# Kernel optimization log

Hardware: AMD Instinct MI355X
Metric: run time of the kernel (lower is better)

## Reference

```python
import jax, jax.numpy as jnp
import numpy as np

N_NODES = 50000


def _sage_mean(x, src, dst, Wl, bl, Wr, n_nodes):
    # PyG SAGEConv (aggr='mean', root_weight=True): lin_l(mean_j x_j) + lin_r(x_i)
    msgs = x[src]                                             # [E, F] gather
    agg = jax.ops.segment_sum(msgs, dst, num_segments=n_nodes)  # [N, F]
    cnt = jax.ops.segment_sum(jnp.ones((src.shape[0],), x.dtype), dst,
                              num_segments=n_nodes)           # [N]
    mean = agg / jnp.maximum(cnt, 1.0)[:, None]
    return mean @ Wl + bl + x @ Wr


def setup_inputs() -> dict:
    key = jax.random.key(0)
    ks = jax.random.split(key, 12)
    in_ft = 64
    o0, o1, o2 = 64, 128, 128
    d2 = o0 + o0          # conv2 in = 128
    d3 = o0 + o0 + o1     # conv3 in = 256
    E = 800000

    def lin(k, fi, fo):
        s = 1.0 / np.sqrt(fi)
        return jax.random.uniform(k, (fi, fo), jnp.float32, -s, s)

    x = jax.random.normal(ks[0], (N_NODES, in_ft), jnp.float32)
    edge_index = jax.random.randint(ks[1], (2, E), 0, N_NODES, jnp.int64)
    return {
        "x": x,
        "edge_index": edge_index,
        "Wp": lin(ks[2], in_ft, o0), "bp": jnp.zeros((o0,), jnp.float32),
        "Wl1": lin(ks[3], in_ft, o0), "bl1": jnp.zeros((o0,), jnp.float32),
        "Wr1": lin(ks[4], in_ft, o0),
        "Wl2": lin(ks[5], d2, o1), "bl2": jnp.zeros((o1,), jnp.float32),
        "Wr2": lin(ks[6], d2, o1),
        "Wl3": lin(ks[7], d3, o2), "bl3": jnp.zeros((o2,), jnp.float32),
        "Wr3": lin(ks[8], d3, o2),
    }


def reference(x, edge_index, Wp, bp, Wl1, bl1, Wr1, Wl2, bl2, Wr2, Wl3, bl3, Wr3):
    src, dst = edge_index[0], edge_index[1]
    act = jax.nn.relu
    x_p = act(x @ Wp + bp)                                        # [N, o0]
    h1 = act(_sage_mean(x, src, dst, Wl1, bl1, Wr1, N_NODES))      # [N, o0]
    in2 = jnp.concatenate([x_p, h1], axis=1)                      # [N, 2*o0]
    h2 = act(_sage_mean(in2, src, dst, Wl2, bl2, Wr2, N_NODES))    # [N, o1]
    in3 = jnp.concatenate([x_p, h1, h2], axis=1)                  # [N, 2*o0+o1]
    h3 = act(_sage_mean(in3, src, dst, Wl3, bl3, Wr3, N_NODES))    # [N, o2]
    return h3
```

## Files before the change

kernel.cpp:

```cpp
#include <hip/hip_runtime.h>

#define N_NODES 50000
#define ELLW 48

typedef unsigned int uint;
typedef unsigned short ushort;
typedef float floatx4 __attribute__((ext_vector_type(4)));
typedef short short8 __attribute__((ext_vector_type(8)));

__device__ inline ushort f2bf(float f) {
    uint u = __float_as_uint(f);
    return (ushort)((u + 0x7fffu + ((u >> 16) & 1u)) >> 16);
}
__device__ inline float bflo(uint u) { return __uint_as_float(u << 16); }
__device__ inline float bfhi(uint u) { return __uint_as_float(u & 0xffff0000u); }


__device__ inline void swz_body(const float* __restrict__ W, ushort* __restrict__ Wz,
                                int O, int t) {
    int lane = t & 63, cb = t >> 6;
    int NBm = O / 16;
    int c = cb / NBm, nb = cb % NBm;
    int quad = lane >> 4, l16 = lane & 15;
#pragma unroll
    for (int j = 0; j < 8; j++) {
        float v = W[(size_t)(c * 32 + quad * 8 + j) * O + nb * 16 + l16];
        Wz[(size_t)t * 8 + j] = f2bf(v);
    }
}

__device__ void gemm1_body(int gb, const float* __restrict__ x,
                           const float* __restrict__ Wp, const float* __restrict__ bp,
                           ushort* __restrict__ feats, ushort* ldsA) {
    constexpr int LDA = 40;
    const int tid = threadIdx.x;
    const int wave = tid >> 6, lane = tid & 63;
    const int quad = lane >> 4, l16 = lane & 15;
    const int node0 = gb * 64;

    floatx4 acc[4];
#pragma unroll
    for (int nb = 0; nb < 4; nb++) acc[nb] = (floatx4){0.f, 0.f, 0.f, 0.f};

#pragma unroll
    for (int kk = 0; kk < 2; kk++) {
        const int k0 = kk * 32;
        __syncthreads();
        {
            int row = tid >> 2, seg = tid & 3;
            int node = node0 + row;
            float4 v0 = {0.f,0.f,0.f,0.f}, v1 = {0.f,0.f,0.f,0.f};
            if (node < N_NODES) {
                v0 = *(const float4*)&x[(size_t)node * 64 + k0 + seg * 8];
                v1 = *(const float4*)&x[(size_t)node * 64 + k0 + seg * 8 + 4];
            }
            ushort4 o0, o1;
            o0.x = f2bf(v0.x); o0.y = f2bf(v0.y); o0.z = f2bf(v0.z); o0.w = f2bf(v0.w);
            o1.x = f2bf(v1.x); o1.y = f2bf(v1.y); o1.z = f2bf(v1.z); o1.w = f2bf(v1.w);
            *(ushort4*)&ldsA[row * LDA + seg * 8] = o0;
            *(ushort4*)&ldsA[row * LDA + seg * 8 + 4] = o1;
        }
        __syncthreads();

        short8 a = *(const short8*)&ldsA[(wave * 16 + l16) * LDA + quad * 8];
#pragma unroll
        for (int nb = 0; nb < 4; nb++) {
            short8 bfrag;
#pragma unroll
            for (int j = 0; j < 8; j++)
                bfrag[j] = (short)f2bf(Wp[(size_t)(k0 + quad * 8 + j) * 64 + nb * 16 + l16]);
            acc[nb] = __builtin_amdgcn_mfma_f32_16x16x32_bf16(a, bfrag, acc[nb], 0, 0, 0);
        }
    }

#pragma unroll
    for (int nb = 0; nb < 4; nb++) {
        int ncol = nb * 16 + l16;
        float bv = bp[ncol];
#pragma unroll
        for (int r = 0; r < 4; r++) {
            int node = node0 + wave * 16 + quad * 4 + r;
            if (node >= N_NODES) continue;
            float v = fmaxf(acc[nb][r] + bv, 0.f);
            feats[(size_t)node * 256 + ncol] = f2bf(v);
        }
    }
}

__global__ __launch_bounds__(256) void k1_mega(
    const int* __restrict__ src, const int* __restrict__ dst, int E,
    int* __restrict__ fillc, ushort* __restrict__ ell,
    const float* __restrict__ x, ushort* __restrict__ xb,
    const float* __restrict__ Wp, const float* __restrict__ bp, ushort* __restrict__ feats,
    const float* __restrict__ Wl1, ushort* __restrict__ zl1,
    const float* __restrict__ Wr1, ushort* __restrict__ zr1,
    const float* __restrict__ Wl2, ushort* __restrict__ zl2,
    const float* __restrict__ Wr2, ushort* __restrict__ zr2,
    const float* __restrict__ Wl3, ushort* __restrict__ zl3,
    const float* __restrict__ Wr3, ushort* __restrict__ zr3,
    int NF, int NG, int NC)
{
    __shared__ ushort ldsA[64 * 40];
    int b = blockIdx.x, tid = threadIdx.x;
    if (b < NF) {
        int t = b * 256 + tid;
        if (t < E) {
            int d = dst[t], s = src[t];
            int p = atomicAdd(&fillc[d], 1);
            if (p < ELLW) ell[(size_t)d * ELLW + p] = (ushort)s;
        }
        return;
    }
    b -= NF;
    if (b < NG) { gemm1_body(b, x, Wp, bp, feats, ldsA); return; }
    b -= NG;
    if (b < NC) {
        int t = b * 256 + tid;
        float4 v = ((const float4*)x)[t];
        ushort4 o;
        o.x = f2bf(v.x); o.y = f2bf(v.y); o.z = f2bf(v.z); o.w = f2bf(v.w);
        ((ushort4*)xb)[t] = o;
        return;
    }
    b -= NC;
    if      (b < 2)  swz_body(Wl1, zl1, 64,  (b - 0) * 256 + tid);
    else if (b < 4)  swz_body(Wr1, zr1, 64,  (b - 2) * 256 + tid);
    else if (b < 12) swz_body(Wl2, zl2, 128, (b - 4) * 256 + tid);
    else if (b < 20) swz_body(Wr2, zr2, 128, (b - 12) * 256 + tid);
    else if (b < 36) swz_body(Wl3, zl3, 128, (b - 20) * 256 + tid);
    else             swz_body(Wr3, zr3, 128, (b - 36) * 256 + tid);
}


__global__ __launch_bounds__(256) void gather64_k(const int* __restrict__ fillc,
                                                  const ushort* __restrict__ ell,
                                                  const ushort* __restrict__ in, int sin,
                                                  ushort* __restrict__ out, int sout) {
    int node = blockIdx.x * 4 + (threadIdx.x >> 6);
    if (node >= N_NODES) return;
    int lane = threadIdx.x & 63;
    int sub = lane >> 3, c = lane & 7;
    int n = fillc[node]; int nc = (n > ELLW) ? ELLW : n;
    const ushort* base = ell + (size_t)node * ELLW;
    float a[8];
#pragma unroll
    for (int j = 0; j < 8; j++) a[j] = 0.f;

    int i = sub;
    for (; i + 8 < nc; i += 16) {
        uint4 u0 = *(const uint4*)&in[(size_t)base[i] * sin + 8 * c];
        uint4 u1 = *(const uint4*)&in[(size_t)base[i + 8] * sin + 8 * c];
        a[0] += bflo(u0.x) + bflo(u1.x);  a[1] += bfhi(u0.x) + bfhi(u1.x);
        a[2] += bflo(u0.y) + bflo(u1.y);  a[3] += bfhi(u0.y) + bfhi(u1.y);
        a[4] += bflo(u0.z) + bflo(u1.z);  a[5] += bfhi(u0.z) + bfhi(u1.z);
        a[6] += bflo(u0.w) + bflo(u1.w);  a[7] += bfhi(u0.w) + bfhi(u1.w);
    }
    if (i < nc) {
        uint4 u0 = *(const uint4*)&in[(size_t)base[i] * sin + 8 * c];
        a[0] += bflo(u0.x);  a[1] += bfhi(u0.x);
        a[2] += bflo(u0.y);  a[3] += bfhi(u0.y);
        a[4] += bflo(u0.z);  a[5] += bfhi(u0.z);
        a[6] += bflo(u0.w);  a[7] += bfhi(u0.w);
    }
#pragma unroll
    for (int d = 8; d < 64; d <<= 1)
#pragma unroll
        for (int j = 0; j < 8; j++) a[j] += __shfl_xor(a[j], d);
    if (sub == 0) {
        float iv = 1.0f / fmaxf((float)n, 1.0f);
        uint4 r;
        r.x = (uint)f2bf(a[0] * iv) | ((uint)f2bf(a[1] * iv) << 16);
        r.y = (uint)f2bf(a[2] * iv) | ((uint)f2bf(a[3] * iv) << 16);
        r.z = (uint)f2bf(a[4] * iv) | ((uint)f2bf(a[5] * iv) << 16);
        r.w = (uint)f2bf(a[6] * iv) | ((uint)f2bf(a[7] * iv) << 16);
        *(uint4*)&out[(size_t)node * sout + 8 * c] = r;
    }
}

__global__ __launch_bounds__(256) void gather128_k(const int* __restrict__ fillc,
                                                   const ushort* __restrict__ ell,
                                                   const ushort* __restrict__ in, int sin,
                                                   ushort* __restrict__ out, int sout) {
    int node = blockIdx.x * 4 + (threadIdx.x >> 6);
    if (node >= N_NODES) return;
    int lane = threadIdx.x & 63;
    int sub = lane >> 4, c = lane & 15;
    int n = fillc[node]; int nc = (n > ELLW) ? ELLW : n;
    const ushort* base = ell + (size_t)node * ELLW;
    float a[8];
#pragma unroll
    for (int j = 0; j < 8; j++) a[j] = 0.f;

    int i = sub;
    for (; i + 12 < nc; i += 16) {
        uint4 u0 = *(const uint4*)&in[(size_t)base[i] * sin + 8 * c];
        uint4 u1 = *(const uint4*)&in[(size_t)base[i + 4] * sin + 8 * c];
        uint4 u2 = *(const uint4*)&in[(size_t)base[i + 8] * sin + 8 * c];
        uint4 u3 = *(const uint4*)&in[(size_t)base[i + 12] * sin + 8 * c];
        a[0] += (bflo(u0.x) + bflo(u1.x)) + (bflo(u2.x) + bflo(u3.x));
        a[1] += (bfhi(u0.x) + bfhi(u1.x)) + (bfhi(u2.x) + bfhi(u3.x));
        a[2] += (bflo(u0.y) + bflo(u1.y)) + (bflo(u2.y) + bflo(u3.y));
        a[3] += (bfhi(u0.y) + bfhi(u1.y)) + (bfhi(u2.y) + bfhi(u3.y));
        a[4] += (bflo(u0.z) + bflo(u1.z)) + (bflo(u2.z) + bflo(u3.z));
        a[5] += (bfhi(u0.z) + bfhi(u1.z)) + (bfhi(u2.z) + bfhi(u3.z));
        a[6] += (bflo(u0.w) + bflo(u1.w)) + (bflo(u2.w) + bflo(u3.w));
        a[7] += (bfhi(u0.w) + bfhi(u1.w)) + (bfhi(u2.w) + bfhi(u3.w));
    }
    for (; i < nc; i += 4) {
        uint4 u0 = *(const uint4*)&in[(size_t)base[i] * sin + 8 * c];
        a[0] += bflo(u0.x);  a[1] += bfhi(u0.x);
        a[2] += bflo(u0.y);  a[3] += bfhi(u0.y);
        a[4] += bflo(u0.z);  a[5] += bfhi(u0.z);
        a[6] += bflo(u0.w);  a[7] += bfhi(u0.w);
    }
#pragma unroll
    for (int d = 16; d < 64; d <<= 1)
#pragma unroll
        for (int j = 0; j < 8; j++) a[j] += __shfl_xor(a[j], d);
    if (sub == 0) {
        float iv = 1.0f / fmaxf((float)n, 1.0f);
        uint4 r;
        r.x = (uint)f2bf(a[0] * iv) | ((uint)f2bf(a[1] * iv) << 16);
        r.y = (uint)f2bf(a[2] * iv) | ((uint)f2bf(a[3] * iv) << 16);
        r.z = (uint)f2bf(a[4] * iv) | ((uint)f2bf(a[5] * iv) << 16);
        r.w = (uint)f2bf(a[6] * iv) | ((uint)f2bf(a[7] * iv) << 16);
        *(uint4*)&out[(size_t)node * sout + 8 * c] = r;
    }
}


template <int O, bool OUT_BF16>
__global__ __launch_bounds__(256) void mfma_gemm_k(
    const ushort* __restrict__ A1, int s1, int K1, const ushort* __restrict__ Wz1,
    const ushort* __restrict__ A2, int s2, int K2, const ushort* __restrict__ Wz2,
    const float* __restrict__ bias, void* __restrict__ outp, int so, int ocol)
{
    constexpr int NB = O / 16;
    constexpr int LDA = 40;
    __shared__ ushort ldsA[64 * LDA];

    const int tid = threadIdx.x;
    const int wave = tid >> 6, lane = tid & 63;
    const int quad = lane >> 4, l16 = lane & 15;
    const int node0 = blockIdx.x * 64;

    floatx4 acc[NB];
#pragma unroll
    for (int nb = 0; nb < NB; nb++) acc[nb] = (floatx4){0.f, 0.f, 0.f, 0.f};

#pragma unroll 1
    for (int phase = 0; phase < 2; ++phase) {
        const ushort* A = phase ? A2 : A1;
        const ushort* Wz = phase ? Wz2 : Wz1;
        const int K = phase ? K2 : K1;
        const int sA = phase ? s2 : s1;

#pragma unroll 1
        for (int k0 = 0; k0 < K; k0 += 32) {
            __syncthreads();
            {
                int row = tid >> 2, seg = tid & 3;
                int node = node0 + row;
                uint4 v = {0u, 0u, 0u, 0u};
                if (node < N_NODES)
                    v = *(const uint4*)&A[(size_t)node * sA + k0 + seg * 8];
                *(uint4*)&ldsA[row * LDA + seg * 8] = v;
            }
            __syncthreads();

            short8 a = *(const short8*)&ldsA[(wave * 16 + l16) * LDA + quad * 8];
            const short8* bz = (const short8*)Wz + (size_t)(k0 >> 5) * NB * 64;
#pragma unroll
            for (int nb = 0; nb < NB; nb++) {
                short8 b = bz[nb * 64 + lane];
                acc[nb] = __builtin_amdgcn_mfma_f32_16x16x32_bf16(a, b, acc[nb], 0, 0, 0);
            }
        }
    }

#pragma unroll
    for (int nb = 0; nb < NB; nb++) {
        int ncol = nb * 16 + l16;
        float bv = bias[ncol];
#pragma unroll
        for (int r = 0; r < 4; r++) {
            int node = node0 + wave * 16 + quad * 4 + r;
            if (node >= N_NODES) continue;
            float v = fmaxf(acc[nb][r] + bv, 0.f);
            if (OUT_BF16)
                ((ushort*)outp)[(size_t)node * so + ocol + ncol] = f2bf(v);
            else
                ((float*)outp)[(size_t)node * so + ocol + ncol] = v;
        }
    }
}


extern "C" void kernel_launch(void* const* d_in, const int* in_sizes, int n_in,
                              void* d_out, int out_size, void* d_ws, size_t ws_size,
                              hipStream_t stream) {
    const float* x   = (const float*)d_in[0];
    const int*   ei  = (const int*)d_in[1];
    const float* Wp  = (const float*)d_in[2];
    const float* bp  = (const float*)d_in[3];
    const float* Wl1 = (const float*)d_in[4];
    const float* bl1 = (const float*)d_in[5];
    const float* Wr1 = (const float*)d_in[6];
    const float* Wl2 = (const float*)d_in[7];
    const float* bl2 = (const float*)d_in[8];
    const float* Wr2 = (const float*)d_in[9];
    const float* Wl3 = (const float*)d_in[10];
    const float* bl3 = (const float*)d_in[11];
    const float* Wr3 = (const float*)d_in[12];

    const int E = in_sizes[1] / 2;
    const int N = N_NODES;
    const int* src = ei;
    const int* dst = ei + E;

    char* p = (char*)d_ws;
    ushort* xb    = (ushort*)p;  p += (size_t)N * 64 * 2;
    ushort* feats = (ushort*)p;  p += (size_t)N * 256 * 2;
    ushort* aggx  = (ushort*)p;  p += (size_t)N * 64 * 2;
    ushort* aggf  = (ushort*)p;  p += (size_t)N * 256 * 2;
    int* fillc    = (int*)p;     p += (size_t)N * 4;
    ushort* ell   = (ushort*)p;  p += (size_t)N * ELLW * 2;
    ushort* zl1   = (ushort*)p;  p += 64 * 64 * 2;
    ushort* zr1   = (ushort*)p;  p += 64 * 64 * 2;
    ushort* zl2   = (ushort*)p;  p += 128 * 128 * 2;
    ushort* zr2   = (ushort*)p;  p += 128 * 128 * 2;
    ushort* zl3   = (ushort*)p;  p += 256 * 128 * 2;
    ushort* zr3   = (ushort*)p;  p += 256 * 128 * 2;

    hipMemsetAsync(fillc, 0, (size_t)N * sizeof(int), stream);

    const int NF = (E + 255) / 256;
    const int NG = (N + 63) / 64;
    const int NC = (N * 64 / 4) / 256;

    k1_mega<<<NF + NG + NC + 52, 256, 0, stream>>>(
        src, dst, E, fillc, ell, x, xb, Wp, bp, feats,
        Wl1, zl1, Wr1, zr1, Wl2, zl2, Wr2, zr2, Wl3, zl3, Wr3, zr3,
        NF, NG, NC);

    gather64_k<<<(N + 3) / 4, 256, 0, stream>>>(fillc, ell, xb, 64, aggx, 64);

    mfma_gemm_k<64, true><<<NG, 256, 0, stream>>>(
        aggx, 64, 64, zl1, xb, 64, 64, zr1, bl1, feats, 256, 64);

    gather128_k<<<(N + 3) / 4, 256, 0, stream>>>(fillc, ell, feats, 256, aggf, 256);

    mfma_gemm_k<128, true><<<NG, 256, 0, stream>>>(
        aggf, 256, 128, zl2, feats, 256, 128, zr2, bl2, feats, 256, 128);

    gather128_k<<<(N + 3) / 4, 256, 0, stream>>>(fillc, ell, feats + 128, 256, aggf + 128, 256);

    mfma_gemm_k<128, false><<<NG, 256, 0, stream>>>(
        aggf, 256, 256, zl3, feats, 256, 256, zr3, bl3, (float*)d_out, 128, 0);
}
```

Before: 291.4 us.

## Split SAGE GEMMs into root and aggregate parts, overlapping root GEMMs with gathers

Each SAGE layer's `lin_r(x)` term is now computed separately into an fp32 partial buffer. For layer 1 it runs inside the first mega-kernel alongside the `x_p` projection. For layers 2 and 3 it runs in the same launch as the neighbour gather, with gather blocks and GEMM blocks mixed in one grid. The final per-layer kernel then only multiplies the aggregated features by `lin_l` and adds the stored partial, bias and relu. The aim is to hide root-weight GEMM work behind the memory-bound gathers and shorten the critical path. In exchange it adds extra global traffic, because fp32 partials are written and read back for every layer.

```diff
diff --git a/kernel.cpp b/kernel.cpp
--- a/kernel.cpp
+++ b/kernel.cpp
@@ -14,7 +14,6 @@
 }
 __device__ inline float bflo(uint u) { return __uint_as_float(u << 16); }
 __device__ inline float bfhi(uint u) { return __uint_as_float(u & 0xffff0000u); }
-
 
 __device__ inline void swz_body(const float* __restrict__ W, ushort* __restrict__ Wz,
                                 int O, int t) {
@@ -31,16 +30,18 @@
 
 __device__ void gemm1_body(int gb, const float* __restrict__ x,
                            const float* __restrict__ Wp, const float* __restrict__ bp,
-                           ushort* __restrict__ feats, ushort* ldsA) {
+                           const float* __restrict__ Wr1,
+                           ushort* __restrict__ feats, float* __restrict__ P1,
+                           ushort* ldsA) {
     constexpr int LDA = 40;
     const int tid = threadIdx.x;
     const int wave = tid >> 6, lane = tid & 63;
     const int quad = lane >> 4, l16 = lane & 15;
     const int node0 = gb * 64;
 
-    floatx4 acc[4];
-#pragma unroll
-    for (int nb = 0; nb < 4; nb++) acc[nb] = (floatx4){0.f, 0.f, 0.f, 0.f};
+    floatx4 aP[4], aR[4];
+#pragma unroll
+    for (int nb = 0; nb < 4; nb++) { aP[nb] = (floatx4){0,0,0,0}; aR[nb] = (floatx4){0,0,0,0}; }
 
 #pragma unroll
     for (int kk = 0; kk < 2; kk++) {
@@ -49,7 +50,7 @@
         {
             int row = tid >> 2, seg = tid & 3;
             int node = node0 + row;
-            float4 v0 = {0.f,0.f,0.f,0.f}, v1 = {0.f,0.f,0.f,0.f};
+            float4 v0 = {0,0,0,0}, v1 = {0,0,0,0};
             if (node < N_NODES) {
                 v0 = *(const float4*)&x[(size_t)node * 64 + k0 + seg * 8];
                 v1 = *(const float4*)&x[(size_t)node * 64 + k0 + seg * 8 + 4];
@@ -65,11 +66,19 @@
         short8 a = *(const short8*)&ldsA[(wave * 16 + l16) * LDA + quad * 8];
 #pragma unroll
         for (int nb = 0; nb < 4; nb++) {
-            short8 bfrag;
+            short8 bw;
 #pragma unroll
             for (int j = 0; j < 8; j++)
-                bfrag[j] = (short)f2bf(Wp[(size_t)(k0 + quad * 8 + j) * 64 + nb * 16 + l16]);
-            acc[nb] = __builtin_amdgcn_mfma_f32_16x16x32_bf16(a, bfrag, acc[nb], 0, 0, 0);
+                bw[j] = (short)f2bf(Wp[(size_t)(k0 + quad * 8 + j) * 64 + nb * 16 + l16]);
+            aP[nb] = __builtin_amdgcn_mfma_f32_16x16x32_bf16(a, bw, aP[nb], 0, 0, 0);
+        }
+#pragma unroll
+        for (int nb = 0; nb < 4; nb++) {
+            short8 bw;
+#pragma unroll
+            for (int j = 0; j < 8; j++)
+                bw[j] = (short)f2bf(Wr1[(size_t)(k0 + quad * 8 + j) * 64 + nb * 16 + l16]);
+            aR[nb] = __builtin_amdgcn_mfma_f32_16x16x32_bf16(a, bw, aR[nb], 0, 0, 0);
         }
     }
 
@@ -81,8 +90,8 @@
         for (int r = 0; r < 4; r++) {
             int node = node0 + wave * 16 + quad * 4 + r;
             if (node >= N_NODES) continue;
-            float v = fmaxf(acc[nb][r] + bv, 0.f);
-            feats[(size_t)node * 256 + ncol] = f2bf(v);
+            feats[(size_t)node * 256 + ncol] = f2bf(fmaxf(aP[nb][r] + bv, 0.f));
+            P1[(size_t)node * 64 + ncol] = aR[nb][r];
         }
     }
 }
@@ -91,9 +100,9 @@
     const int* __restrict__ src, const int* __restrict__ dst, int E,
     int* __restrict__ fillc, ushort* __restrict__ ell,
     const float* __restrict__ x, ushort* __restrict__ xb,
-    const float* __restrict__ Wp, const float* __restrict__ bp, ushort* __restrict__ feats,
+    const float* __restrict__ Wp, const float* __restrict__ bp,
+    const float* __restrict__ Wr1, ushort* __restrict__ feats, float* __restrict__ P1,
     const float* __restrict__ Wl1, ushort* __restrict__ zl1,
-    const float* __restrict__ Wr1, ushort* __restrict__ zr1,
     const float* __restrict__ Wl2, ushort* __restrict__ zl2,
     const float* __restrict__ Wr2, ushort* __restrict__ zr2,
     const float* __restrict__ Wl3, ushort* __restrict__ zl3,
@@ -112,7 +121,7 @@
         return;
     }
     b -= NF;
-    if (b < NG) { gemm1_body(b, x, Wp, bp, feats, ldsA); return; }
+    if (b < NG) { gemm1_body(b, x, Wp, bp, Wr1, feats, P1, ldsA); return; }
     b -= NG;
     if (b < NC) {
         int t = b * 256 + tid;
@@ -124,18 +133,17 @@
     }
     b -= NC;
     if      (b < 2)  swz_body(Wl1, zl1, 64,  (b - 0) * 256 + tid);
-    else if (b < 4)  swz_body(Wr1, zr1, 64,  (b - 2) * 256 + tid);
-    else if (b < 12) swz_body(Wl2, zl2, 128, (b - 4) * 256 + tid);
-    else if (b < 20) swz_body(Wr2, zr2, 128, (b - 12) * 256 + tid);
-    else if (b < 36) swz_body(Wl3, zl3, 128, (b - 20) * 256 + tid);
-    else             swz_body(Wr3, zr3, 128, (b - 36) * 256 + tid);
+    else if (b < 10) swz_body(Wl2, zl2, 128, (b - 2) * 256 + tid);
+    else if (b < 18) swz_body(Wr2, zr2, 128, (b - 10) * 256 + tid);
+    else if (b < 34) swz_body(Wl3, zl3, 128, (b - 18) * 256 + tid);
+    else             swz_body(Wr3, zr3, 128, (b - 34) * 256 + tid);
 }
 
 
 __global__ __launch_bounds__(256) void gather64_k(const int* __restrict__ fillc,
                                                   const ushort* __restrict__ ell,
-                                                  const ushort* __restrict__ in, int sin,
-                                                  ushort* __restrict__ out, int sout) {
+                                                  const ushort* __restrict__ in,
+                                                  ushort* __restrict__ out) {
     int node = blockIdx.x * 4 + (threadIdx.x >> 6);
     if (node >= N_NODES) return;
     int lane = threadIdx.x & 63;
@@ -148,15 +156,15 @@
 
     int i = sub;
     for (; i + 8 < nc; i += 16) {
-        uint4 u0 = *(const uint4*)&in[(size_t)base[i] * sin + 8 * c];
-        uint4 u1 = *(const uint4*)&in[(size_t)base[i + 8] * sin + 8 * c];
+        uint4 u0 = *(const uint4*)&in[(size_t)base[i] * 64 + 8 * c];
+        uint4 u1 = *(const uint4*)&in[(size_t)base[i + 8] * 64 + 8 * c];
         a[0] += bflo(u0.x) + bflo(u1.x);  a[1] += bfhi(u0.x) + bfhi(u1.x);
         a[2] += bflo(u0.y) + bflo(u1.y);  a[3] += bfhi(u0.y) + bfhi(u1.y);
         a[4] += bflo(u0.z) + bflo(u1.z);  a[5] += bfhi(u0.z) + bfhi(u1.z);
         a[6] += bflo(u0.w) + bflo(u1.w);  a[7] += bfhi(u0.w) + bfhi(u1.w);
     }
     if (i < nc) {
-        uint4 u0 = *(const uint4*)&in[(size_t)base[i] * sin + 8 * c];
+        uint4 u0 = *(const uint4*)&in[(size_t)base[i] * 64 + 8 * c];
         a[0] += bflo(u0.x);  a[1] += bfhi(u0.x);
         a[2] += bflo(u0.y);  a[3] += bfhi(u0.y);
         a[4] += bflo(u0.z);  a[5] += bfhi(u0.z);
@@ -173,15 +181,15 @@
         r.y = (uint)f2bf(a[2] * iv) | ((uint)f2bf(a[3] * iv) << 16);
         r.z = (uint)f2bf(a[4] * iv) | ((uint)f2bf(a[5] * iv) << 16);
         r.w = (uint)f2bf(a[6] * iv) | ((uint)f2bf(a[7] * iv) << 16);
-        *(uint4*)&out[(size_t)node * sout + 8 * c] = r;
-    }
-}
-
-__global__ __launch_bounds__(256) void gather128_k(const int* __restrict__ fillc,
-                                                   const ushort* __restrict__ ell,
-                                                   const ushort* __restrict__ in, int sin,
-                                                   ushort* __restrict__ out, int sout) {
-    int node = blockIdx.x * 4 + (threadIdx.x >> 6);
+        *(uint4*)&out[(size_t)node * 64 + 8 * c] = r;
+    }
+}
+
+__device__ void gather128_body(int gb, const int* __restrict__ fillc,
+                               const ushort* __restrict__ ell,
+                               const ushort* __restrict__ in,
+                               ushort* __restrict__ out) {
+    int node = gb * 4 + (threadIdx.x >> 6);
     if (node >= N_NODES) return;
     int lane = threadIdx.x & 63;
     int sub = lane >> 4, c = lane & 15;
@@ -193,10 +201,10 @@
 
     int i = sub;
     for (; i + 12 < nc; i += 16) {
-        uint4 u0 = *(const uint4*)&in[(size_t)base[i] * sin + 8 * c];
-        uint4 u1 = *(const uint4*)&in[(size_t)base[i + 4] * sin + 8 * c];
-        uint4 u2 = *(const uint4*)&in[(size_t)base[i + 8] * sin + 8 * c];
-        uint4 u3 = *(const uint4*)&in[(size_t)base[i + 12] * sin + 8 * c];
+        uint4 u0 = *(const uint4*)&in[(size_t)base[i] * 256 + 8 * c];
+        uint4 u1 = *(const uint4*)&in[(size_t)base[i + 4] * 256 + 8 * c];
+        uint4 u2 = *(const uint4*)&in[(size_t)base[i + 8] * 256 + 8 * c];
+        uint4 u3 = *(const uint4*)&in[(size_t)base[i + 12] * 256 + 8 * c];
         a[0] += (bflo(u0.x) + bflo(u1.x)) + (bflo(u2.x) + bflo(u3.x));
         a[1] += (bfhi(u0.x) + bfhi(u1.x)) + (bfhi(u2.x) + bfhi(u3.x));
         a[2] += (bflo(u0.y) + bflo(u1.y)) + (bflo(u2.y) + bflo(u3.y));
@@ -207,7 +215,7 @@
         a[7] += (bfhi(u0.w) + bfhi(u1.w)) + (bfhi(u2.w) + bfhi(u3.w));
     }
     for (; i < nc; i += 4) {
-        uint4 u0 = *(const uint4*)&in[(size_t)base[i] * sin + 8 * c];
+        uint4 u0 = *(const uint4*)&in[(size_t)base[i] * 256 + 8 * c];
         a[0] += bflo(u0.x);  a[1] += bfhi(u0.x);
         a[2] += bflo(u0.y);  a[3] += bfhi(u0.y);
         a[4] += bflo(u0.z);  a[5] += bfhi(u0.z);
@@ -224,21 +232,96 @@
         r.y = (uint)f2bf(a[2] * iv) | ((uint)f2bf(a[3] * iv) << 16);
         r.z = (uint)f2bf(a[4] * iv) | ((uint)f2bf(a[5] * iv) << 16);
         r.w = (uint)f2bf(a[6] * iv) | ((uint)f2bf(a[7] * iv) << 16);
-        *(uint4*)&out[(size_t)node * sout + 8 * c] = r;
-    }
-}
-
-
-template <int O, bool OUT_BF16>
-__global__ __launch_bounds__(256) void mfma_gemm_k(
-    const ushort* __restrict__ A1, int s1, int K1, const ushort* __restrict__ Wz1,
-    const ushort* __restrict__ A2, int s2, int K2, const ushort* __restrict__ Wz2,
-    const float* __restrict__ bias, void* __restrict__ outp, int so, int ocol)
+        *(uint4*)&out[(size_t)node * 256 + 8 * c] = r;
+    }
+}
+
+__device__ void pgemm_body(int gb,
+    const ushort* __restrict__ A1, int s1, int o1, int KC1, const ushort* __restrict__ Wz1, int w1,
+    const ushort* __restrict__ A2, int s2, int o2, int KC2, const ushort* __restrict__ Wz2, int w2,
+    float* __restrict__ Pout, ushort* ldsA)
+{
+    constexpr int LDA = 40;
+    const int tid = threadIdx.x;
+    const int wave = tid >> 6, lane = tid & 63;
+    const int quad = lane >> 4, l16 = lane & 15;
+    const int node0 = gb * 64;
+
+    floatx4 acc[8];
+#pragma unroll
+    for (int nb = 0; nb < 8; nb++) acc[nb] = (floatx4){0,0,0,0};
+
+#pragma unroll 1
+    for (int ph = 0; ph < 2; ph++) {
+        const ushort* A = ph ? A2 : A1;
+        const int sA = ph ? s2 : s1, oA = ph ? o2 : o1, KC = ph ? KC2 : KC1, w = ph ? w2 : w1;
+        const short8* Wz = (const short8*)(ph ? Wz2 : Wz1);
+#pragma unroll 1
+        for (int kc = 0; kc < KC; kc++) {
+            __syncthreads();
+            {
+                int row = tid >> 2, seg = tid & 3;
+                int node = node0 + row;
+                uint4 v = {0,0,0,0};
+                if (node < N_NODES)
+                    v = *(const uint4*)&A[(size_t)node * sA + oA + kc * 32 + seg * 8];
+                *(uint4*)&ldsA[row * LDA + seg * 8] = v;
+            }
+            __syncthreads();
+            short8 a = *(const short8*)&ldsA[(wave * 16 + l16) * LDA + quad * 8];
+            const short8* bz = Wz + (size_t)(w + kc) * 8 * 64;
+#pragma unroll
+            for (int nb = 0; nb < 8; nb++)
+                acc[nb] = __builtin_amdgcn_mfma_f32_16x16x32_bf16(a, bz[nb * 64 + lane], acc[nb], 0, 0, 0);
+        }
+    }
+#pragma unroll
+    for (int nb = 0; nb < 8; nb++) {
+        int ncol = nb * 16 + l16;
+#pragma unroll
+        for (int r = 0; r < 4; r++) {
+            int node = node0 + wave * 16 + quad * 4 + r;
+            if (node >= N_NODES) continue;
+            Pout[(size_t)node * 128 + ncol] = acc[nb][r];
+        }
+    }
+}
+
+__global__ __launch_bounds__(256) void mix_a(
+    const int* __restrict__ fillc, const ushort* __restrict__ ell,
+    const ushort* __restrict__ feats, ushort* __restrict__ aggf,
+    const ushort* __restrict__ zr2, float* __restrict__ P2, int NGat)
+{
+    __shared__ ushort ldsA[64 * 40];
+    int b = blockIdx.x;
+    if (b < NGat) { gather128_body(b, fillc, ell, feats, aggf); return; }
+    pgemm_body(b - NGat, feats, 256, 0, 4, zr2, 0,
+               feats, 256, 0, 0, zr2, 0, P2, ldsA);
+}
+
+__global__ __launch_bounds__(256) void mix_b(
+    const int* __restrict__ fillc, const ushort* __restrict__ ell,
+    const ushort* __restrict__ feats, ushort* __restrict__ aggf,
+    const ushort* __restrict__ zr3, const ushort* __restrict__ zl3,
+    float* __restrict__ P3, int NGat)
+{
+    __shared__ ushort ldsA[64 * 40];
+    int b = blockIdx.x;
+    if (b < NGat) { gather128_body(b, fillc, ell, feats + 128, aggf + 128); return; }
+    pgemm_body(b - NGat, feats, 256, 0, 8, zr3, 0,
+               aggf, 256, 0, 4, zl3, 0, P3, ldsA);
+}
+
+template <int O, int KC, bool OUT_BF16>
+__global__ __launch_bounds__(256) void final_k(
+    const ushort* __restrict__ A, int sA, int aofs,
+    const ushort* __restrict__ Wz, int wofs,
+    const float* __restrict__ part, const float* __restrict__ bias,
+    void* __restrict__ outp, int so, int ocol)
 {
     constexpr int NB = O / 16;
     constexpr int LDA = 40;
     __shared__ ushort ldsA[64 * LDA];
-
     const int tid = threadIdx.x;
     const int wave = tid >> 6, lane = tid & 63;
     const int quad = lane >> 4, l16 = lane & 15;
@@ -246,36 +329,25 @@
 
     floatx4 acc[NB];
 #pragma unroll
-    for (int nb = 0; nb < NB; nb++) acc[nb] = (floatx4){0.f, 0.f, 0.f, 0.f};
+    for (int nb = 0; nb < NB; nb++) acc[nb] = (floatx4){0,0,0,0};
 
 #pragma unroll 1
-    for (int phase = 0; phase < 2; ++phase) {
-        const ushort* A = phase ? A2 : A1;
-        const ushort* Wz = phase ? Wz2 : Wz1;
-        const int K = phase ? K2 : K1;
-        const int sA = phase ? s2 : s1;
-
-#pragma unroll 1
-        for (int k0 = 0; k0 < K; k0 += 32) {
-            __syncthreads();
-            {
-                int row = tid >> 2, seg = tid & 3;
-                int node = node0 + row;
-                uint4 v = {0u, 0u, 0u, 0u};
-                if (node < N_NODES)
-                    v = *(const uint4*)&A[(size_t)node * sA + k0 + seg * 8];
-                *(uint4*)&ldsA[row * LDA + seg * 8] = v;
-            }
-            __syncthreads();
-
-            short8 a = *(const short8*)&ldsA[(wave * 16 + l16) * LDA + quad * 8];
-            const short8* bz = (const short8*)Wz + (size_t)(k0 >> 5) * NB * 64;
-#pragma unroll
-            for (int nb = 0; nb < NB; nb++) {
-                short8 b = bz[nb * 64 + lane];
-                acc[nb] = __builtin_amdgcn_mfma_f32_16x16x32_bf16(a, b, acc[nb], 0, 0, 0);
-            }
-        }
+    for (int kc = 0; kc < KC; kc++) {
+        __syncthreads();
+        {
+            int row = tid >> 2, seg = tid & 3;
+            int node = node0 + row;
+            uint4 v = {0,0,0,0};
+            if (node < N_NODES)
+                v = *(const uint4*)&A[(size_t)node * sA + aofs + kc * 32 + seg * 8];
+            *(uint4*)&ldsA[row * LDA + seg * 8] = v;
+        }
+        __syncthreads();
+        short8 a = *(const short8*)&ldsA[(wave * 16 + l16) * LDA + quad * 8];
+        const short8* bz = (const short8*)Wz + (size_t)(wofs + kc) * NB * 64;
+#pragma unroll
+        for (int nb = 0; nb < NB; nb++)
+            acc[nb] = __builtin_amdgcn_mfma_f32_16x16x32_bf16(a, bz[nb * 64 + lane], acc[nb], 0, 0, 0);
     }
 
 #pragma unroll
@@ -286,7 +358,7 @@
         for (int r = 0; r < 4; r++) {
             int node = node0 + wave * 16 + quad * 4 + r;
             if (node >= N_NODES) continue;
-            float v = fmaxf(acc[nb][r] + bv, 0.f);
+            float v = fmaxf(acc[nb][r] + part[(size_t)node * O + ncol] + bv, 0.f);
             if (OUT_BF16)
                 ((ushort*)outp)[(size_t)node * so + ocol + ncol] = f2bf(v);
             else
@@ -325,8 +397,9 @@
     ushort* aggf  = (ushort*)p;  p += (size_t)N * 256 * 2;
     int* fillc    = (int*)p;     p += (size_t)N * 4;
     ushort* ell   = (ushort*)p;  p += (size_t)N * ELLW * 2;
+    float* P1     = (float*)p;   p += (size_t)N * 64 * 4;
+    float* P23    = (float*)p;   p += (size_t)N * 128 * 4;
     ushort* zl1   = (ushort*)p;  p += 64 * 64 * 2;
-    ushort* zr1   = (ushort*)p;  p += 64 * 64 * 2;
     ushort* zl2   = (ushort*)p;  p += 128 * 128 * 2;
     ushort* zr2   = (ushort*)p;  p += 128 * 128 * 2;
     ushort* zl3   = (ushort*)p;  p += 256 * 128 * 2;
@@ -334,27 +407,28 @@
 
     hipMemsetAsync(fillc, 0, (size_t)N * sizeof(int), stream);
 
-    const int NF = (E + 255) / 256;
-    const int NG = (N + 63) / 64;
-    const int NC = (N * 64 / 4) / 256;
-
-    k1_mega<<<NF + NG + NC + 52, 256, 0, stream>>>(
-        src, dst, E, fillc, ell, x, xb, Wp, bp, feats,
-        Wl1, zl1, Wr1, zr1, Wl2, zl2, Wr2, zr2, Wl3, zl3, Wr3, zr3,
+    const int NF   = (E + 255) / 256;
+    const int NG   = (N + 63) / 64;
+    const int NC   = (N * 64 / 4) / 256;
+    const int NGat = (N + 3) / 4;
+
+    k1_mega<<<NF + NG + NC + 50, 256, 0, stream>>>(
+        src, dst, E, fillc, ell, x, xb, Wp, bp, Wr1, feats, P1,
+        Wl1, zl1, Wl2, zl2, Wr2, zr2, Wl3, zl3, Wr3, zr3,
         NF, NG, NC);
 
-    gather64_k<<<(N + 3) / 4, 256, 0, stream>>>(fillc, ell, xb, 64, aggx, 64);
-
-    mfma_gemm_k<64, true><<<NG, 256, 0, stream>>>(
-        aggx, 64, 64, zl1, xb, 64, 64, zr1, bl1, feats, 256, 64);
-
-    gather128_k<<<(N + 3) / 4, 256, 0, stream>>>(fillc, ell, feats, 256, aggf, 256);
-
-    mfma_gemm_k<128, true><<<NG, 256, 0, stream>>>(
-        aggf, 256, 128, zl2, feats, 256, 128, zr2, bl2, feats, 256, 128);
-
-    gather128_k<<<(N + 3) / 4, 256, 0, stream>>>(fillc, ell, feats + 128, 256, aggf + 128, 256);
-
-    mfma_gemm_k<128, false><<<NG, 256, 0, stream>>>(
-        aggf, 256, 256, zl3, feats, 256, 256, zr3, bl3, (float*)d_out, 128, 0);
-}
+    gather64_k<<<NGat, 256, 0, stream>>>(fillc, ell, xb, aggx);
+
+    final_k<64, 2, true><<<NG, 256, 0, stream>>>(
+        aggx, 64, 0, zl1, 0, P1, bl1, feats, 256, 64);
+
+    mix_a<<<NGat + NG, 256, 0, stream>>>(fillc, ell, feats, aggf, zr2, P23, NGat);
+
+    final_k<128, 4, true><<<NG, 256, 0, stream>>>(
+        aggf, 256, 0, zl2, 0, P23, bl2, feats, 256, 128);
+
+    mix_b<<<NGat + NG, 256, 0, stream>>>(fillc, ell, feats, aggf, zr3, zl3, P23, NGat);
+
+    final_k<128, 4, false><<<NG, 256, 0, stream>>>(
+        aggf, 256, 128, zl3, 4, P23, bl3, (float*)d_out, 128, 0);
+}
```

New measurement: 339.8 us. 1.17x slower.

## Bin edges by destination range before ELL scatter; two nodes per wave in gather64

Applied to the files above, without the earlier changes.

Edges are first bucketed into 8 destination-range bins using block-local LDS counters and one global atomic per bin per block. A new scatter kernel then fills the ELL lists bin by bin, so the atomics on fill counters land on a narrower address range with better locality. The fillc memset moves into the mega kernel, and gather64 now processes two nodes per wave with 32 lanes each. The cost is an extra kernel launch and a round trip through the bin buffer, and a bin overflows if more than 131072 edges share one destination range.

```diff
diff --git a/kernel.cpp b/kernel.cpp
--- a/kernel.cpp
+++ b/kernel.cpp
@@ -2,6 +2,7 @@
 
 #define N_NODES 50000
 #define ELLW 48
+#define BINCAP 131072
 
 typedef unsigned int uint;
 typedef unsigned short ushort;
@@ -14,7 +15,6 @@
 }
 __device__ inline float bflo(uint u) { return __uint_as_float(u << 16); }
 __device__ inline float bfhi(uint u) { return __uint_as_float(u & 0xffff0000u); }
-
 
 __device__ inline void swz_body(const float* __restrict__ W, ushort* __restrict__ Wz,
                                 int O, int t) {
@@ -40,7 +40,7 @@
 
     floatx4 acc[4];
 #pragma unroll
-    for (int nb = 0; nb < 4; nb++) acc[nb] = (floatx4){0.f, 0.f, 0.f, 0.f};
+    for (int nb = 0; nb < 4; nb++) acc[nb] = (floatx4){0, 0, 0, 0};
 
 #pragma unroll
     for (int kk = 0; kk < 2; kk++) {
@@ -49,7 +49,7 @@
         {
             int row = tid >> 2, seg = tid & 3;
             int node = node0 + row;
-            float4 v0 = {0.f,0.f,0.f,0.f}, v1 = {0.f,0.f,0.f,0.f};
+            float4 v0 = {0, 0, 0, 0}, v1 = {0, 0, 0, 0};
             if (node < N_NODES) {
                 v0 = *(const float4*)&x[(size_t)node * 64 + k0 + seg * 8];
                 v1 = *(const float4*)&x[(size_t)node * 64 + k0 + seg * 8 + 4];
@@ -65,11 +65,11 @@
         short8 a = *(const short8*)&ldsA[(wave * 16 + l16) * LDA + quad * 8];
 #pragma unroll
         for (int nb = 0; nb < 4; nb++) {
-            short8 bfrag;
+            short8 bw;
 #pragma unroll
             for (int j = 0; j < 8; j++)
-                bfrag[j] = (short)f2bf(Wp[(size_t)(k0 + quad * 8 + j) * 64 + nb * 16 + l16]);
-            acc[nb] = __builtin_amdgcn_mfma_f32_16x16x32_bf16(a, bfrag, acc[nb], 0, 0, 0);
+                bw[j] = (short)f2bf(Wp[(size_t)(k0 + quad * 8 + j) * 64 + nb * 16 + l16]);
+            acc[nb] = __builtin_amdgcn_mfma_f32_16x16x32_bf16(a, bw, acc[nb], 0, 0, 0);
         }
     }
 
@@ -81,15 +81,14 @@
         for (int r = 0; r < 4; r++) {
             int node = node0 + wave * 16 + quad * 4 + r;
             if (node >= N_NODES) continue;
-            float v = fmaxf(acc[nb][r] + bv, 0.f);
-            feats[(size_t)node * 256 + ncol] = f2bf(v);
+            feats[(size_t)node * 256 + ncol] = f2bf(fmaxf(acc[nb][r] + bv, 0.f));
         }
     }
 }
 
 __global__ __launch_bounds__(256) void k1_mega(
     const int* __restrict__ src, const int* __restrict__ dst, int E,
-    int* __restrict__ fillc, ushort* __restrict__ ell,
+    uint* __restrict__ bins, int* __restrict__ binCnt, int* __restrict__ fillc,
     const float* __restrict__ x, ushort* __restrict__ xb,
     const float* __restrict__ Wp, const float* __restrict__ bp, ushort* __restrict__ feats,
     const float* __restrict__ Wl1, ushort* __restrict__ zl1,
@@ -98,20 +97,29 @@
     const float* __restrict__ Wr2, ushort* __restrict__ zr2,
     const float* __restrict__ Wl3, ushort* __restrict__ zl3,
     const float* __restrict__ Wr3, ushort* __restrict__ zr3,
-    int NF, int NG, int NC)
+    int NA, int NG, int NC, int NZ)
 {
     __shared__ ushort ldsA[64 * 40];
+    __shared__ int cnt[8], base[8];
     int b = blockIdx.x, tid = threadIdx.x;
-    if (b < NF) {
+
+    if (b < NA) {
         int t = b * 256 + tid;
-        if (t < E) {
-            int d = dst[t], s = src[t];
-            int p = atomicAdd(&fillc[d], 1);
-            if (p < ELLW) ell[(size_t)d * ELLW + p] = (ushort)s;
-        }
+        bool valid = t < E;
+        int s = 0, d = 0, bin = 0;
+        if (valid) { s = src[t]; d = dst[t]; bin = d / 6250; }
+        if (tid < 8) cnt[tid] = 0;
+        __syncthreads();
+        int rank = 0;
+        if (valid) rank = atomicAdd(&cnt[bin], 1);
+        __syncthreads();
+        if (tid < 8) base[tid] = atomicAdd(&binCnt[tid], cnt[tid]);
+        __syncthreads();
+        if (valid)
+            bins[(size_t)bin * BINCAP + base[bin] + rank] = (uint)s | ((uint)d << 16);
         return;
     }
-    b -= NF;
+    b -= NA;
     if (b < NG) { gemm1_body(b, x, Wp, bp, feats, ldsA); return; }
     b -= NG;
     if (b < NC) {
@@ -123,6 +131,12 @@
         return;
     }
     b -= NC;
+    if (b < NZ) {
+        int t = b * 256 + tid;
+        if (t < 12500) ((uint4*)fillc)[t] = (uint4){0, 0, 0, 0};
+        return;
+    }
+    b -= NZ;
     if      (b < 2)  swz_body(Wl1, zl1, 64,  (b - 0) * 256 + tid);
     else if (b < 4)  swz_body(Wr1, zr1, 64,  (b - 2) * 256 + tid);
     else if (b < 12) swz_body(Wl2, zl2, 128, (b - 4) * 256 + tid);
@@ -131,15 +145,34 @@
     else             swz_body(Wr3, zr3, 128, (b - 36) * 256 + tid);
 }
 
+__global__ __launch_bounds__(256) void scatter_k(const uint* __restrict__ bins,
+                                                 const int* __restrict__ binCnt,
+                                                 int* __restrict__ fillc,
+                                                 ushort* __restrict__ ell) {
+    int bin = blockIdx.x & 7;
+    int sub = blockIdx.x >> 3;
+    int n = binCnt[bin];
+    const uint* bp = bins + (size_t)bin * BINCAP;
+    for (int i = sub * 256 + threadIdx.x; i < n; i += 64 * 256) {
+        uint pk = bp[i];
+        int s = pk & 0xFFFF, d = pk >> 16;
+        int p = atomicAdd(&fillc[d], 1);
+        if (p < ELLW) ell[(size_t)d * ELLW + p] = (ushort)s;
+    }
+}
+
 
 __global__ __launch_bounds__(256) void gather64_k(const int* __restrict__ fillc,
                                                   const ushort* __restrict__ ell,
-                                                  const ushort* __restrict__ in, int sin,
-                                                  ushort* __restrict__ out, int sout) {
-    int node = blockIdx.x * 4 + (threadIdx.x >> 6);
+                                                  const ushort* __restrict__ in,
+                                                  ushort* __restrict__ out) {
+    int wid = blockIdx.x * 4 + (threadIdx.x >> 6);
+    int lane = threadIdx.x & 63;
+    int half = lane >> 5;
+    int node = wid * 2 + half;
     if (node >= N_NODES) return;
-    int lane = threadIdx.x & 63;
-    int sub = lane >> 3, c = lane & 7;
+    int l32 = lane & 31;
+    int sub = l32 >> 3, c = l32 & 7;
     int n = fillc[node]; int nc = (n > ELLW) ? ELLW : n;
     const ushort* base = ell + (size_t)node * ELLW;
     float a[8];
@@ -147,56 +180,11 @@
     for (int j = 0; j < 8; j++) a[j] = 0.f;
 
     int i = sub;
-    for (; i + 8 < nc; i += 16) {
-        uint4 u0 = *(const uint4*)&in[(size_t)base[i] * sin + 8 * c];
-        uint4 u1 = *(const uint4*)&in[(size_t)base[i + 8] * sin + 8 * c];
-        a[0] += bflo(u0.x) + bflo(u1.x);  a[1] += bfhi(u0.x) + bfhi(u1.x);
-        a[2] += bflo(u0.y) + bflo(u1.y);  a[3] += bfhi(u0.y) + bfhi(u1.y);
-        a[4] += bflo(u0.z) + bflo(u1.z);  a[5] += bfhi(u0.z) + bfhi(u1.z);
-        a[6] += bflo(u0.w) + bflo(u1.w);  a[7] += bfhi(u0.w) + bfhi(u1.w);
-    }
-    if (i < nc) {
-        uint4 u0 = *(const uint4*)&in[(size_t)base[i] * sin + 8 * c];
-        a[0] += bflo(u0.x);  a[1] += bfhi(u0.x);
-        a[2] += bflo(u0.y);  a[3] += bfhi(u0.y);
-        a[4] += bflo(u0.z);  a[5] += bfhi(u0.z);
-        a[6] += bflo(u0.w);  a[7] += bfhi(u0.w);
-    }
-#pragma unroll
-    for (int d = 8; d < 64; d <<= 1)
-#pragma unroll
-        for (int j = 0; j < 8; j++) a[j] += __shfl_xor(a[j], d);
-    if (sub == 0) {
-        float iv = 1.0f / fmaxf((float)n, 1.0f);
-        uint4 r;
-        r.x = (uint)f2bf(a[0] * iv) | ((uint)f2bf(a[1] * iv) << 16);
-        r.y = (uint)f2bf(a[2] * iv) | ((uint)f2bf(a[3] * iv) << 16);
-        r.z = (uint)f2bf(a[4] * iv) | ((uint)f2bf(a[5] * iv) << 16);
-        r.w = (uint)f2bf(a[6] * iv) | ((uint)f2bf(a[7] * iv) << 16);
-        *(uint4*)&out[(size_t)node * sout + 8 * c] = r;
-    }
-}
-
-__global__ __launch_bounds__(256) void gather128_k(const int* __restrict__ fillc,
-                                                   const ushort* __restrict__ ell,
-                                                   const ushort* __restrict__ in, int sin,
-                                                   ushort* __restrict__ out, int sout) {
-    int node = blockIdx.x * 4 + (threadIdx.x >> 6);
-    if (node >= N_NODES) return;
-    int lane = threadIdx.x & 63;
-    int sub = lane >> 4, c = lane & 15;
-    int n = fillc[node]; int nc = (n > ELLW) ? ELLW : n;
-    const ushort* base = ell + (size_t)node * ELLW;
-    float a[8];
-#pragma unroll
-    for (int j = 0; j < 8; j++) a[j] = 0.f;
-
-    int i = sub;
     for (; i + 12 < nc; i += 16) {
-        uint4 u0 = *(const uint4*)&in[(size_t)base[i] * sin + 8 * c];
-        uint4 u1 = *(const uint4*)&in[(size_t)base[i + 4] * sin + 8 * c];
-        uint4 u2 = *(const uint4*)&in[(size_t)base[i + 8] * sin + 8 * c];
-        uint4 u3 = *(const uint4*)&in[(size_t)base[i + 12] * sin + 8 * c];
+        uint4 u0 = *(const uint4*)&in[(size_t)base[i] * 64 + 8 * c];
+        uint4 u1 = *(const uint4*)&in[(size_t)base[i + 4] * 64 + 8 * c];
+        uint4 u2 = *(const uint4*)&in[(size_t)base[i + 8] * 64 + 8 * c];
+        uint4 u3 = *(const uint4*)&in[(size_t)base[i + 12] * 64 + 8 * c];
         a[0] += (bflo(u0.x) + bflo(u1.x)) + (bflo(u2.x) + bflo(u3.x));
         a[1] += (bfhi(u0.x) + bfhi(u1.x)) + (bfhi(u2.x) + bfhi(u3.x));
         a[2] += (bflo(u0.y) + bflo(u1.y)) + (bflo(u2.y) + bflo(u3.y));
@@ -207,16 +195,17 @@
         a[7] += (bfhi(u0.w) + bfhi(u1.w)) + (bfhi(u2.w) + bfhi(u3.w));
     }
     for (; i < nc; i += 4) {
-        uint4 u0 = *(const uint4*)&in[(size_t)base[i] * sin + 8 * c];
+        uint4 u0 = *(const uint4*)&in[(size_t)base[i] * 64 + 8 * c];
         a[0] += bflo(u0.x);  a[1] += bfhi(u0.x);
         a[2] += bflo(u0.y);  a[3] += bfhi(u0.y);
         a[4] += bflo(u0.z);  a[5] += bfhi(u0.z);
         a[6] += bflo(u0.w);  a[7] += bfhi(u0.w);
     }
 #pragma unroll
-    for (int d = 16; d < 64; d <<= 1)
-#pragma unroll
-        for (int j = 0; j < 8; j++) a[j] += __shfl_xor(a[j], d);
+    for (int j = 0; j < 8; j++) {
+        a[j] += __shfl_xor(a[j], 8);
+        a[j] += __shfl_xor(a[j], 16);
+    }
     if (sub == 0) {
         float iv = 1.0f / fmaxf((float)n, 1.0f);
         uint4 r;
@@ -224,7 +213,59 @@
         r.y = (uint)f2bf(a[2] * iv) | ((uint)f2bf(a[3] * iv) << 16);
         r.z = (uint)f2bf(a[4] * iv) | ((uint)f2bf(a[5] * iv) << 16);
         r.w = (uint)f2bf(a[6] * iv) | ((uint)f2bf(a[7] * iv) << 16);
-        *(uint4*)&out[(size_t)node * sout + 8 * c] = r;
+        *(uint4*)&out[(size_t)node * 64 + 8 * c] = r;
+    }
+}
+
+__global__ __launch_bounds__(256) void gather128_k(const int* __restrict__ fillc,
+                                                   const ushort* __restrict__ ell,
+                                                   const ushort* __restrict__ in,
+                                                   ushort* __restrict__ out) {
+    int node = blockIdx.x * 4 + (threadIdx.x >> 6);
+    if (node >= N_NODES) return;
+    int lane = threadIdx.x & 63;
+    int sub = lane >> 4, c = lane & 15;
+    int n = fillc[node]; int nc = (n > ELLW) ? ELLW : n;
+    const ushort* base = ell + (size_t)node * ELLW;
+    float a[8];
+#pragma unroll
+    for (int j = 0; j < 8; j++) a[j] = 0.f;
+
+    int i = sub;
+    for (; i + 12 < nc; i += 16) {
+        uint4 u0 = *(const uint4*)&in[(size_t)base[i] * 256 + 8 * c];
+        uint4 u1 = *(const uint4*)&in[(size_t)base[i + 4] * 256 + 8 * c];
+        uint4 u2 = *(const uint4*)&in[(size_t)base[i + 8] * 256 + 8 * c];
+        uint4 u3 = *(const uint4*)&in[(size_t)base[i + 12] * 256 + 8 * c];
+        a[0] += (bflo(u0.x) + bflo(u1.x)) + (bflo(u2.x) + bflo(u3.x));
+        a[1] += (bfhi(u0.x) + bfhi(u1.x)) + (bfhi(u2.x) + bfhi(u3.x));
+        a[2] += (bflo(u0.y) + bflo(u1.y)) + (bflo(u2.y) + bflo(u3.y));
+        a[3] += (bfhi(u0.y) + bfhi(u1.y)) + (bfhi(u2.y) + bfhi(u3.y));
+        a[4] += (bflo(u0.z) + bflo(u1.z)) + (bflo(u2.z) + bflo(u3.z));
+        a[5] += (bfhi(u0.z) + bfhi(u1.z)) + (bfhi(u2.z) + bfhi(u3.z));
+        a[6] += (bflo(u0.w) + bflo(u1.w)) + (bflo(u2.w) + bflo(u3.w));
+        a[7] += (bfhi(u0.w) + bfhi(u1.w)) + (bfhi(u2.w) + bfhi(u3.w));
+    }
+    for (; i < nc; i += 4) {
+        uint4 u0 = *(const uint4*)&in[(size_t)base[i] * 256 + 8 * c];
+        a[0] += bflo(u0.x);  a[1] += bfhi(u0.x);
+        a[2] += bflo(u0.y);  a[3] += bfhi(u0.y);
+        a[4] += bflo(u0.z);  a[5] += bfhi(u0.z);
+        a[6] += bflo(u0.w);  a[7] += bfhi(u0.w);
+    }
+#pragma unroll
+    for (int j = 0; j < 8; j++) {
+        a[j] += __shfl_xor(a[j], 16);
+        a[j] += __shfl_xor(a[j], 32);
+    }
+    if (sub == 0) {
+        float iv = 1.0f / fmaxf((float)n, 1.0f);
+        uint4 r;
+        r.x = (uint)f2bf(a[0] * iv) | ((uint)f2bf(a[1] * iv) << 16);
+        r.y = (uint)f2bf(a[2] * iv) | ((uint)f2bf(a[3] * iv) << 16);
+        r.z = (uint)f2bf(a[4] * iv) | ((uint)f2bf(a[5] * iv) << 16);
+        r.w = (uint)f2bf(a[6] * iv) | ((uint)f2bf(a[7] * iv) << 16);
+        *(uint4*)&out[(size_t)node * 256 + 8 * c] = r;
     }
 }
 
@@ -246,7 +287,7 @@
 
     floatx4 acc[NB];
 #pragma unroll
-    for (int nb = 0; nb < NB; nb++) acc[nb] = (floatx4){0.f, 0.f, 0.f, 0.f};
+    for (int nb = 0; nb < NB; nb++) acc[nb] = (floatx4){0, 0, 0, 0};
 
 #pragma unroll 1
     for (int phase = 0; phase < 2; ++phase) {
@@ -261,7 +302,7 @@
             {
                 int row = tid >> 2, seg = tid & 3;
                 int node = node0 + row;
-                uint4 v = {0u, 0u, 0u, 0u};
+                uint4 v = {0, 0, 0, 0};
                 if (node < N_NODES)
                     v = *(const uint4*)&A[(size_t)node * sA + k0 + seg * 8];
                 *(uint4*)&ldsA[row * LDA + seg * 8] = v;
@@ -325,6 +366,8 @@
     ushort* aggf  = (ushort*)p;  p += (size_t)N * 256 * 2;
     int* fillc    = (int*)p;     p += (size_t)N * 4;
     ushort* ell   = (ushort*)p;  p += (size_t)N * ELLW * 2;
+    uint* bins    = (uint*)p;    p += (size_t)8 * BINCAP * 4;
+    int* binCnt   = (int*)p;     p += 16 * 4;
     ushort* zl1   = (ushort*)p;  p += 64 * 64 * 2;
     ushort* zr1   = (ushort*)p;  p += 64 * 64 * 2;
     ushort* zl2   = (ushort*)p;  p += 128 * 128 * 2;
@@ -332,28 +375,31 @@
     ushort* zl3   = (ushort*)p;  p += 256 * 128 * 2;
     ushort* zr3   = (ushort*)p;  p += 256 * 128 * 2;
 
-    hipMemsetAsync(fillc, 0, (size_t)N * sizeof(int), stream);
-
-    const int NF = (E + 255) / 256;
+    hipMemsetAsync(binCnt, 0, 16 * sizeof(int), stream);
+
+    const int NA = (E + 255) / 256;
     const int NG = (N + 63) / 64;
     const int NC = (N * 64 / 4) / 256;
-
-    k1_mega<<<NF + NG + NC + 52, 256, 0, stream>>>(
-        src, dst, E, fillc, ell, x, xb, Wp, bp, feats,
+    const int NZ = 49;
+
+    k1_mega<<<NA + NG + NC + NZ + 52, 256, 0, stream>>>(
+        src, dst, E, bins, binCnt, fillc, x, xb, Wp, bp, feats,
         Wl1, zl1, Wr1, zr1, Wl2, zl2, Wr2, zr2, Wl3, zl3, Wr3, zr3,
-        NF, NG, NC);
-
-    gather64_k<<<(N + 3) / 4, 256, 0, stream>>>(fillc, ell, xb, 64, aggx, 64);
+        NA, NG, NC, NZ);
+
+    scatter_k<<<512, 256, 0, stream>>>(bins, binCnt, fillc, ell);
+
+    gather64_k<<<(N + 7) / 8, 256, 0, stream>>>(fillc, ell, xb, aggx);
 
     mfma_gemm_k<64, true><<<NG, 256, 0, stream>>>(
         aggx, 64, 64, zl1, xb, 64, 64, zr1, bl1, feats, 256, 64);
 
-    gather128_k<<<(N + 3) / 4, 256, 0, stream>>>(fillc, ell, feats, 256, aggf, 256);
+    gather128_k<<<(N + 3) / 4, 256, 0, stream>>>(fillc, ell, feats, aggf);
 
     mfma_gemm_k<128, true><<<NG, 256, 0, stream>>>(
         aggf, 256, 128, zl2, feats, 256, 128, zr2, bl2, feats, 256, 128);
 
-    gather128_k<<<(N + 3) / 4, 256, 0, stream>>>(fillc, ell, feats + 128, 256, aggf + 128, 256);
+    gather128_k<<<(N + 3) / 4, 256, 0, stream>>>(fillc, ell, feats + 128, aggf + 128);
 
     mfma_gemm_k<128, false><<<NG, 256, 0, stream>>>(
         aggf, 256, 256, zl3, feats, 256, 256, zr3, bl3, (float*)d_out, 128, 0);
```

Result: slower. 306.7 us (+5.3%).
